# Optimization experiments

Measured on AMD Instinct MI355X. Metric: run time of the kernel, lower is better.

Reference implementation:

```python
import jax, jax.numpy as jnp
import numpy as np

IMG = 800          # image size (square)
STRIDE = 4         # feature-map stride
S = 14             # rcnn_crop_size
C = 256            # crop_channels
N = 512            # number of rpn proposals
NUM_CLASSES = 81   # COCO (incl. background at index 0)
HID = 1024
NMS_TH = 0.5
SCORE_TH = 0.05


def setup_inputs() -> dict:
    key = jax.random.key(0)
    ks = jax.random.split(key, 8)
    features = jax.random.normal(ks[0], (1, C, IMG // STRIDE, IMG // STRIDE), jnp.float32)
    # valid proposal boxes (x0, y0, x1, y1) in image coordinates
    u = jax.random.uniform(ks[1], (N, 4), jnp.float32)
    x0 = u[:, 0] * (IMG - 64.0)
    y0 = u[:, 1] * (IMG - 64.0)
    bw = 16.0 + u[:, 2] * 240.0
    bh = 16.0 + u[:, 3] * 240.0
    proposals = jnp.stack([x0, y0, jnp.minimum(x0 + bw, IMG - 1.0), jnp.minimum(y0 + bh, IMG - 1.0)], axis=1)
    d1 = C * S * S  # 50176
    w1 = jax.random.normal(ks[2], (d1, HID), jnp.float32) * (1.0 / np.sqrt(d1))
    b1 = jnp.zeros((HID,), jnp.float32)
    w2 = jax.random.normal(ks[3], (HID, HID), jnp.float32) * (1.0 / np.sqrt(HID))
    b2 = jnp.zeros((HID,), jnp.float32)
    w_cls = jax.random.normal(ks[4], (HID, NUM_CLASSES), jnp.float32) * (1.0 / np.sqrt(HID))
    b_cls = jnp.zeros((NUM_CLASSES,), jnp.float32)
    w_reg = jax.random.normal(ks[5], (HID, NUM_CLASSES * 4), jnp.float32) * (1.0 / np.sqrt(HID))
    b_reg = jnp.zeros((NUM_CLASSES * 4,), jnp.float32)
    return dict(features=features, proposals=proposals, w1=w1, b1=b1, w2=w2, b2=b2,
                w_cls=w_cls, b_cls=b_cls, w_reg=w_reg, b_reg=b_reg)


def roi_align(feat, boxes):
    """feat: [C,H,W]; boxes: [N,4] image coords -> crops [N,C,S,S] via bilinear sampling (1 sample per bin)."""
    _, H, W = feat.shape
    b = boxes / STRIDE
    t = (jnp.arange(S, dtype=feat.dtype) + 0.5) / S                # [S] bin centers
    xs = b[:, 0:1] + (b[:, 2:3] - b[:, 0:1]) * t                   # [N,S]
    ys = b[:, 1:2] + (b[:, 3:4] - b[:, 1:2]) * t                   # [N,S]
    xx = jnp.broadcast_to(xs[:, None, :], (boxes.shape[0], S, S))  # [N,S,S]
    yy = jnp.broadcast_to(ys[:, :, None], (boxes.shape[0], S, S))
    x0f = jnp.floor(xx); y0f = jnp.floor(yy)
    fx = xx - x0f; fy = yy - y0f
    x0i = jnp.clip(x0f.astype(jnp.int32), 0, W - 1); x1i = jnp.clip(x0i + 1, 0, W - 1)
    y0i = jnp.clip(y0f.astype(jnp.int32), 0, H - 1); y1i = jnp.clip(y0i + 1, 0, H - 1)
    # gathers -> [C,N,S,S]
    v = (((1 - fx) * (1 - fy))[None] * feat[:, y0i, x0i]
         + (fx * (1 - fy))[None] * feat[:, y0i, x1i]
         + ((1 - fx) * fy)[None] * feat[:, y1i, x0i]
         + (fx * fy)[None] * feat[:, y1i, x1i])
    return v.transpose(1, 0, 2, 3)  # [N,C,S,S]


def decode_boxes(rois, d):
    w = rois[:, 2] - rois[:, 0]; h = rois[:, 3] - rois[:, 1]
    cx = rois[:, 0] + 0.5 * w; cy = rois[:, 1] + 0.5 * h
    px = cx + d[:, 0] * w; py = cy + d[:, 1] * h
    pw = w * jnp.exp(jnp.clip(d[:, 2], -4.0, 4.0))
    ph = h * jnp.exp(jnp.clip(d[:, 3], -4.0, 4.0))
    b = jnp.stack([px - 0.5 * pw, py - 0.5 * ph, px + 0.5 * pw, py + 0.5 * ph], axis=1)
    return jnp.clip(b, 0.0, IMG - 1.0)


def iou_matrix(b):
    area = jnp.maximum(b[:, 2] - b[:, 0], 0.0) * jnp.maximum(b[:, 3] - b[:, 1], 0.0)
    ix0 = jnp.maximum(b[:, None, 0], b[None, :, 0])
    iy0 = jnp.maximum(b[:, None, 1], b[None, :, 1])
    ix1 = jnp.minimum(b[:, None, 2], b[None, :, 2])
    iy1 = jnp.minimum(b[:, None, 3], b[None, :, 3])
    inter = jnp.maximum(ix1 - ix0, 0.0) * jnp.maximum(iy1 - iy0, 0.0)
    return inter / (area[:, None] + area[None, :] - inter + 1e-6)


def reference(features, proposals, w1, b1, w2, b2, w_cls, b_cls, w_reg, b_reg):
    # 1) RoIAlign crop
    crops = roi_align(features[0], proposals)              # [N,C,S,S]
    # 2) RCNN head
    x = crops.reshape(N, -1)
    x = jax.nn.relu(x @ w1 + b1)
    x = jax.nn.relu(x @ w2 + b2)
    logits = x @ w_cls + b_cls                             # [N,81]
    deltas = (x @ w_reg + b_reg).reshape(N, NUM_CLASSES, 4)
    # 3) NMS post-processing
    probs = jax.nn.softmax(logits, axis=-1)
    fg = probs[:, 1:]                                      # exclude background
    labels = jnp.argmax(fg, axis=-1) + 1                   # [N]
    scores = jnp.max(fg, axis=-1)                          # [N]
    d = deltas[jnp.arange(N), labels]                      # per-ROI delta of predicted class
    boxes = decode_boxes(proposals, d)
    order = jnp.argsort(-scores)
    bs = boxes[order]; ss = scores[order]; ls = labels[order]
    valid = ss > SCORE_TH
    M = iou_matrix(bs)                                     # [N,N]
    idx = jnp.arange(N)
    def body(i, keep):
        alive = keep[i] & valid[i]
        supp = (M[i] > NMS_TH) & (idx > i) & alive
        return keep & (~supp)
    keep = jax.lax.fori_loop(0, N, body, valid)
    keepf = jax.lax.stop_gradient(keep.astype(bs.dtype))
    final = jnp.concatenate([bs, ss[:, None]], axis=1) * keepf[:, None]   # [N,5]
    return final, ls.astype(jnp.int32), keep
```

## Files before the change

### kernel.cpp

```cpp
#include <hip/hip_runtime.h>
#include <cstdint>

#define F_H 200
#define F_W 200
#define D1  50176
#define NBOX 512
#define NHID 1024

typedef _Float16 f16;
typedef _Float16 half8 __attribute__((ext_vector_type(8)));
typedef _Float16 half4v __attribute__((ext_vector_type(4)));
typedef _Float16 half2v __attribute__((ext_vector_type(2)));
typedef float    f32x4 __attribute__((ext_vector_type(4)));

__device__ __forceinline__ void gload16(const void* g, void* l) {
  __builtin_amdgcn_global_load_lds((const __attribute__((address_space(1))) void*)g,
                                   (__attribute__((address_space(3))) void*)l,
                                   16, 0, 0);
}

__device__ __forceinline__ half2v pkrtz(float a, float b) {
  return __builtin_bit_cast(half2v, __builtin_amdgcn_cvt_pkrtz(a, b));
}

__device__ __forceinline__ void splitf16(float v, f16& h, f16& l) {
  f16 hh = (f16)v;
  float hf = (float)hh;
  if (fabsf(hf) < 6.1035156e-5f) hf = 0.f;
  h = (f16)hh;
  if (fabsf(hf) < 6.1035156e-5f) h = (f16)0.f;
  l = (f16)((v - hf) * 2048.f);
}

__global__ __launch_bounds__(256) void k_roi(const float* __restrict__ feat,
                                             const float* __restrict__ prop,
                                             f16* __restrict__ xhi, f16* __restrict__ xlo) {
  uint32_t idx = blockIdx.x * 256u + threadIdx.x;
  uint32_t n = idx / 25088u;
  uint32_t rem = idx % 25088u;
  uint32_t c = rem / 98u;
  uint32_t r2 = rem % 98u;
  uint32_t i = r2 / 7u;
  uint32_t jp = r2 % 7u;
  float b0 = prop[n * 4 + 0] * 0.25f, b1 = prop[n * 4 + 1] * 0.25f;
  float b2 = prop[n * 4 + 2] * 0.25f, b3 = prop[n * 4 + 3] * 0.25f;
  float ty = ((float)i + 0.5f) * (1.0f / 14.0f);
  float yy = b1 + (b3 - b1) * ty;
  float y0f = floorf(yy);
  float fy = yy - y0f;
  int y0 = (int)y0f; y0 = y0 < 0 ? 0 : (y0 > F_H - 1 ? F_H - 1 : y0);
  int y1 = y0 + 1 > F_H - 1 ? F_H - 1 : y0 + 1;
  const float* fr0 = feat + (size_t)c * (F_H * F_W) + (size_t)y0 * F_W;
  const float* fr1 = feat + (size_t)c * (F_H * F_W) + (size_t)y1 * F_W;
  f16 hs[2], ls[2];
#pragma unroll
  for (int e = 0; e < 2; ++e) {
    uint32_t j = jp * 2u + (uint32_t)e;
    float tx = ((float)j + 0.5f) * (1.0f / 14.0f);
    float xx = b0 + (b2 - b0) * tx;
    float x0f = floorf(xx);
    float fx = xx - x0f;
    int x0 = (int)x0f; x0 = x0 < 0 ? 0 : (x0 > F_W - 1 ? F_W - 1 : x0);
    int x1 = x0 + 1 > F_W - 1 ? F_W - 1 : x0 + 1;
    float v00 = fr0[x0], v01 = fr0[x1], v10 = fr1[x0], v11 = fr1[x1];
    float v = (1.f - fx) * (1.f - fy) * v00 + fx * (1.f - fy) * v01 +
              (1.f - fx) * fy * v10 + fx * fy * v11;
    splitf16(v, hs[e], ls[e]);
  }
  uint32_t base = n * 50176u + c * 196u + i * 14u + jp * 2u;
  half2v hv; hv[0] = hs[0]; hv[1] = hs[1];
  half2v lv; lv[0] = ls[0]; lv[1] = ls[1];
  *(half2v*)(xhi + base) = hv;
  *(half2v*)(xlo + base) = lv;
}

__global__ __launch_bounds__(256) void k_tsplit(const float* __restrict__ W,
                                                f16* __restrict__ hiT, f16* __restrict__ loT,
                                                int Kdim, int Ndim) {
  __shared__ f16 lh[64 * 72];
  __shared__ f16 ll[64 * 72];
  int t = threadIdx.x;
  int k0 = blockIdx.x * 64, n0 = blockIdx.y * 64;
  int r = t >> 2, cq = t & 3;
  const float* src = W + (size_t)(k0 + r) * Ndim + n0 + cq * 16;
  f16 hv[16], lv[16];
#pragma unroll
  for (int e = 0; e < 4; ++e) {
    f32x4 v = *(const f32x4*)(src + e * 4);
#pragma unroll
    for (int x = 0; x < 4; ++x) splitf16(v[x], hv[e * 4 + x], lv[e * 4 + x]);
  }
#pragma unroll
  for (int j = 0; j < 16; ++j) {
    int n_l = cq * 16 + j;
    lh[n_l * 72 + r] = hv[j];
    ll[n_l * 72 + r] = lv[j];
  }
  __syncthreads();
  f16* oh = hiT + (size_t)(n0 + r) * Kdim + k0 + cq * 16;
  f16* ol = loT + (size_t)(n0 + r) * Kdim + k0 + cq * 16;
  *(half8*)(oh)     = *(const half8*)(&lh[r * 72 + cq * 16]);
  *(half8*)(oh + 8) = *(const half8*)(&lh[r * 72 + cq * 16 + 8]);
  *(half8*)(ol)     = *(const half8*)(&ll[r * 72 + cq * 16]);
  *(half8*)(ol + 8) = *(const half8*)(&ll[r * 72 + cq * 16 + 8]);
}

__global__ __launch_bounds__(256) void k_packT(const float* __restrict__ wc_, const float* __restrict__ bc,
                                               const float* __restrict__ wr_, const float* __restrict__ br,
                                               f16* __restrict__ whT_hi, f16* __restrict__ whT_lo,
                                               float* __restrict__ bh) {
  uint32_t idx = blockIdx.x * 256u + threadIdx.x;
  if (idx < 512u * 1024u) {
    uint32_t n = idx >> 10, k = idx & 1023u;
    float v = 0.f;
    if (n < 81u) v = wc_[k * 81u + n];
    else if (n < 405u) v = wr_[k * 324u + (n - 81u)];
    f16 h, l; splitf16(v, h, l);
    whT_hi[idx] = h; whT_lo[idx] = l;
  } else if (idx < 512u * 1024u + 512u) {
    uint32_t n = idx - 512u * 1024u;
    float v = 0.f;
    if (n < 81u) v = bc[n];
    else if (n < 405u) v = br[n - 81u];
    bh[n] = v;
  }
}

__global__ __launch_bounds__(256) void k_pack(const float* __restrict__ wc, const float* __restrict__ bc,
                                              const float* __restrict__ wr, const float* __restrict__ br,
                                              float* __restrict__ wh, float* __restrict__ bh) {
  uint32_t idx = blockIdx.x * 256u + threadIdx.x;
  if (idx < (uint32_t)NHID * 512u) {
    uint32_t k = idx >> 9, n = idx & 511u;
    float v = 0.f;
    if (n < 81u) v = wc[k * 81u + n];
    else if (n < 405u) v = wr[k * 324u + (n - 81u)];
    wh[idx] = v;
  } else if (idx < (uint32_t)NHID * 512u + 512u) {
    uint32_t n = idx - (uint32_t)NHID * 512u;
    float v = 0.f;
    if (n < 81u) v = bc[n];
    else if (n < 405u) v = br[n - 81u];
    bh[n] = v;
  }
}

__global__ __launch_bounds__(512, 2) void k_gemm2(
    const f16* __restrict__ Ahi, const f16* __restrict__ Alo,
    const f16* __restrict__ Bhi, const f16* __restrict__ Blo,
    float* __restrict__ Cp, int K, int N, int Kc, int nMt, int nNt)
{
  __shared__ char sm[131072];
  const int t = threadIdx.x;
  const int lane = t & 63;
  const int wid = t >> 6;
  const int wr = wid >> 2;
  const int wc = wid & 3;
  const int rl = lane & 15;
  const int lq = lane >> 4;

  int bid = blockIdx.x;
  int low = bid & 7, qq = bid >> 3;
  int nt = qq % nNt;
  int chi = qq / nNt;
  int c = chi * 8 + low;
  int ks = c / nMt;
  int mt = c % nMt;
  const int brow = mt * 256;
  const int nbase = nt * 256;
  const int k0 = ks * Kc;
  const int nk = Kc >> 5;

  uint32_t aoffg[2], aldso[2];
#pragma unroll
  for (int i = 0; i < 2; ++i) {
    uint32_t idx = (uint32_t)t + 512u * i;
    uint32_t q2 = idx >> 2, s = idx & 3;
    uint32_t qh = q2 >> 6;
    uint32_t grh = (qh == 1u) ? 2u : (qh == 2u) ? 1u : qh;
    uint32_t gr = grh * 64u + (q2 & 63u);
    aoffg[i] = (uint32_t)(brow + gr) * (uint32_t)K + (s ^ ((q2 >> 1) & 3u)) * 8u;
    aldso[i] = idx * 16u;
  }
  uint32_t boffg[2], bldso[2];
#pragma unroll
  for (int i = 0; i < 2; ++i) {
    uint32_t idx = (uint32_t)t + 512u * i;
    uint32_t rB = idx >> 2, s = idx & 3;
    boffg[i] = (uint32_t)(nbase + rB) * (uint32_t)K + (s ^ ((rB >> 1) & 3u)) * 8u;
    bldso[i] = idx * 16u;
  }

  const uint32_t swzk = (uint32_t)(lq ^ ((rl >> 1) & 3)) * 16u;
  const uint32_t a_off_lane = (uint32_t)(rl * 64) + swzk;
  const uint32_t b_off_lane = (uint32_t)((wc * 16 + rl) * 64) + swzk;

  f32x4 zero4 = {0.f, 0.f, 0.f, 0.f};
  f32x4 acc[8][4];
#pragma unroll
  for (int m = 0; m < 8; ++m)
#pragma unroll
    for (int n = 0; n < 4; ++n) acc[m][n] = zero4;

#define PH0STAGE(LB, KB) do { \
    gload16(Bhi + boffg[0] + (KB), (LB) + 32768 + bldso[0]); \
    gload16(Blo + boffg[0] + (KB), (LB) + 49152 + bldso[0]); \
    gload16(Bhi + boffg[1] + (KB), (LB) + 32768 + bldso[1]); \
    gload16(Blo + boffg[1] + (KB), (LB) + 49152 + bldso[1]); \
    gload16(Ahi + aoffg[0] + (KB), (LB) + aldso[0]); \
    gload16(Alo + aoffg[0] + (KB), (LB) + 16384 + aldso[0]); \
  } while (0)

#define PH1STAGE(LB, KB) do { \
    gload16(Ahi + aoffg[1] + (KB), (LB) + aldso[1]); \
    gload16(Alo + aoffg[1] + (KB), (LB) + 16384 + aldso[1]); \
  } while (0)

#define COMPUTE_PHASE(P) do { \
    half8 bh2[4], bl2[4]; \
    _Pragma("unroll") \
    for (int nf = 0; nf < 4; ++nf) { \
      bh2[nf] = *(const half8*)(lb + 32768 + nf * 4096 + b_off_lane); \
      bl2[nf] = *(const half8*)(lb + 49152 + nf * 4096 + b_off_lane); \
    } \
    __builtin_amdgcn_s_setprio(1); \
    _Pragma("unroll") \
    for (int mm = 0; mm < 4; ++mm) { \
      const char* ab = lb + (P) * 8192 + wr * 4096 + mm * 1024 + a_off_lane; \
      half8 ah = *(const half8*)(ab); \
      half8 al = *(const half8*)(ab + 16384); \
      _Pragma("unroll") \
      for (int nf = 0; nf < 4; ++nf) { \
        acc[(P)*4+mm][nf] = __builtin_amdgcn_mfma_f32_16x16x32_f16(ah, bh2[nf], acc[(P)*4+mm][nf], 0, 0, 0); \
        f32x4 tt = __builtin_amdgcn_mfma_f32_16x16x32_f16(ah, bl2[nf], zero4, 0, 0, 0); \
        tt = __builtin_amdgcn_mfma_f32_16x16x32_f16(al, bh2[nf], tt, 0, 0, 0); \
        acc[(P)*4+mm][nf] += tt * 4.8828125e-4f; \
      } \
    } \
    __builtin_amdgcn_s_setprio(0); \
  } while (0)

  PH0STAGE(sm, (uint32_t)k0);
  PH1STAGE(sm, (uint32_t)k0);

  int cur = 0;
  for (int kt = 0; kt < nk; ++kt) {
    int ktn = (kt + 1 < nk) ? kt + 1 : kt;
    uint32_t kbn = (uint32_t)(k0 + ktn * 32);
    const char* lb = sm + cur * 65536;
    char* lbn = sm + (cur ^ 1) * 65536;

    asm volatile("s_waitcnt vmcnt(2)" ::: "memory");
    __builtin_amdgcn_s_barrier();
    __builtin_amdgcn_sched_barrier(0);
    PH0STAGE(lbn, kbn);
    COMPUTE_PHASE(0);

    asm volatile("s_waitcnt vmcnt(6)" ::: "memory");
    __builtin_amdgcn_s_barrier();
    __builtin_amdgcn_sched_barrier(0);
    PH1STAGE(lbn, kbn);
    COMPUTE_PHASE(1);

    cur ^= 1;
  }

  float* Cs = Cp + (size_t)ks * ((size_t)512 * (uint32_t)N);
#pragma unroll
  for (int m = 0; m < 8; ++m) {
    int rg = brow + wr * 128 + m * 16 + lq * 4;
#pragma unroll
    for (int nf = 0; nf < 4; ++nf) {
      int cg = nbase + nf * 64 + wc * 16 + rl;
#pragma unroll
      for (int rr = 0; rr < 4; ++rr)
        Cs[(size_t)(rg + rr) * (uint32_t)N + cg] = acc[m][nf][rr];
    }
  }
#undef PH0STAGE
#undef PH1STAGE
#undef COMPUTE_PHASE
}

__global__ __launch_bounds__(512, 2) void k_gemm(
    const f16* __restrict__ Ahi, const f16* __restrict__ Alo,
    const float* __restrict__ B, float* __restrict__ Cp,
    int K, int N, int Kc, int nMt, int nNt)
{
  __shared__ char sm[131072];
  const int t = threadIdx.x;
  const int lane = t & 63;
  const int wid = t >> 6;
  const int wr = wid >> 2;
  const int wc = wid & 3;
  const int rl = lane & 15;
  const int lq = lane >> 4;

  int bid = blockIdx.x;
  int low = bid & 7, q = bid >> 3;
  int nt = q % nNt;
  int chi = q / nNt;
  int c = chi * 8 + low;
  int ks = c / nMt;
  int mt = c % nMt;
  const int brow = mt * 256;
  const int nbase = nt * 256;
  const int k0 = ks * Kc;
  const int nk = Kc >> 5;

  uint32_t aoffg[2], aldso[2];
#pragma unroll
  for (int i = 0; i < 2; ++i) {
    uint32_t idx = (uint32_t)t + 512u * i;
    uint32_t r = idx >> 2, s = idx & 3;
    uint32_t sz = s ^ ((r >> 1) & 3);
    aoffg[i] = (uint32_t)(brow + r) * (uint32_t)K + sz * 8u;
    aldso[i] = idx * 16u;
  }
  uint32_t boffg[2][2], bldso[2][2];
#pragma unroll
  for (int h = 0; h < 2; ++h)
#pragma unroll
    for (int i = 0; i < 2; ++i) {
      uint32_t idx = (uint32_t)t + 512u * i;
      uint32_t kr = idx >> 5, sg = idx & 31;
      uint32_t sgs = sg ^ (((kr >> 3) & 3) << 2);
      boffg[h][i] = kr * (uint32_t)N + (uint32_t)(nbase + h * 128) + sgs * 4u;
      bldso[h][i] = 32768u + (uint32_t)h * 16384u + idx * 16u;
    }

  const uint32_t a_off = (uint32_t)(wr * 8192 + rl * 64) + (uint32_t)((lq ^ ((rl >> 1) & 3)) * 16);
  const uint32_t b_lane = (uint32_t)((((wc ^ lq) & 3) * 16 + rl) * 4);

  f32x4 zero4 = {0.f, 0.f, 0.f, 0.f};
  f32x4 acc[8][4];
#pragma unroll
  for (int m = 0; m < 8; ++m)
#pragma unroll
    for (int n = 0; n < 4; ++n) acc[m][n] = zero4;

#define STAGE_A(LB, KB) do { \
    gload16(Ahi + aoffg[0] + (KB), (LB) + aldso[0]); \
    gload16(Alo + aoffg[0] + (KB), (LB) + 16384 + aldso[0]); \
    gload16(Ahi + aoffg[1] + (KB), (LB) + aldso[1]); \
    gload16(Alo + aoffg[1] + (KB), (LB) + 16384 + aldso[1]); \
  } while (0)

#define STAGE_B(LB, KB) do { \
    gload16(B + (size_t)(KB) * (uint32_t)N + boffg[0][0], (LB) + bldso[0][0]); \
    gload16(B + (size_t)(KB) * (uint32_t)N + boffg[0][1], (LB) + bldso[0][1]); \
    gload16(B + (size_t)(KB) * (uint32_t)N + boffg[1][0], (LB) + bldso[1][0]); \
    gload16(B + (size_t)(KB) * (uint32_t)N + boffg[1][1], (LB) + bldso[1][1]); \
  } while (0)

#define COMPUTE_PHASE(P) do { \
    half8 bhv[2], blv[2]; \
    _Pragma("unroll") \
    for (int x = 0; x < 2; ++x) { \
      const int nf = 2 * (P) + x; \
      const char* bb = lb + 32768 + (nf >> 1) * 16384 + (nf & 1) * 256 + b_lane; \
      _Pragma("unroll") \
      for (int jj = 0; jj < 8; jj += 2) { \
        float v0 = *(const float*)(bb + (lq * 8 + jj) * 512); \
        float v1 = *(const float*)(bb + (lq * 8 + jj + 1) * 512); \
        half2v hp = pkrtz(v0, v1); \
        f16 e0 = (fabsf(v0) >= 6.1035156e-5f) ? hp[0] : (f16)0; \
        f16 e1 = (fabsf(v1) >= 6.1035156e-5f) ? hp[1] : (f16)0; \
        half2v lp = pkrtz((v0 - (float)e0) * 2048.f, (v1 - (float)e1) * 2048.f); \
        bhv[x][jj] = e0; bhv[x][jj + 1] = e1; \
        blv[x][jj] = lp[0]; blv[x][jj + 1] = lp[1]; \
      } \
    } \
    __builtin_amdgcn_s_setprio(1); \
    _Pragma("unroll") \
    for (int m = 0; m < 8; ++m) { \
      half8 ah = *(const half8*)(lb + a_off + m * 1024); \
      half8 al = *(const half8*)(lb + 16384 + a_off + m * 1024); \
      _Pragma("unroll") \
      for (int x = 0; x < 2; ++x) { \
        const int nf = 2 * (P) + x; \
        acc[m][nf] = __builtin_amdgcn_mfma_f32_16x16x32_f16(ah, bhv[x], acc[m][nf], 0, 0, 0); \
        f32x4 tt = __builtin_amdgcn_mfma_f32_16x16x32_f16(ah, blv[x], zero4, 0, 0, 0); \
        tt = __builtin_amdgcn_mfma_f32_16x16x32_f16(al, bhv[x], tt, 0, 0, 0); \
        acc[m][nf] += tt * 4.8828125e-4f; \
      } \
    } \
    __builtin_amdgcn_s_setprio(0); \
  } while (0)

  STAGE_A(sm, (uint32_t)k0);
  STAGE_B(sm, (uint32_t)k0);

  int cur = 0;
  for (int kt = 0; kt < nk; ++kt) {
    int ktn = (kt + 1 < nk) ? kt + 1 : kt;
    uint32_t kbn = (uint32_t)(k0 + ktn * 32);
    const char* lb = sm + cur * 65536;
    char* lbn = sm + (cur ^ 1) * 65536;

    asm volatile("s_waitcnt vmcnt(2)" ::: "memory");
    __builtin_amdgcn_s_barrier();
    __builtin_amdgcn_sched_barrier(0);
    STAGE_A(lbn, kbn);
    COMPUTE_PHASE(0);

    asm volatile("s_waitcnt vmcnt(4)" ::: "memory");
    __builtin_amdgcn_s_barrier();
    __builtin_amdgcn_sched_barrier(0);
    STAGE_B(lbn, kbn);
    COMPUTE_PHASE(1);

    cur ^= 1;
  }

  float* Cs = Cp + (size_t)ks * ((size_t)512 * (uint32_t)N);
#pragma unroll
  for (int m = 0; m < 8; ++m) {
    int rg = brow + wr * 128 + m * 16 + lq * 4;
#pragma unroll
    for (int nf = 0; nf < 4; ++nf) {
      int cg = nbase + nf * 64 + wc * 16 + rl;
#pragma unroll
      for (int rr = 0; rr < 4; ++rr)
        Cs[(size_t)(rg + rr) * (uint32_t)N + cg] = acc[m][nf][rr];
    }
  }
#undef STAGE_A
#undef STAGE_B
#undef COMPUTE_PHASE
}

__global__ __launch_bounds__(256) void k_reduce(
    const float* __restrict__ parts, const float* __restrict__ bias,
    int nS, int MN4, int Ncols, int relu,
    float* __restrict__ outf, f16* __restrict__ ohi, f16* __restrict__ olo)
{
  uint32_t idx = blockIdx.x * 256u + threadIdx.x;
  if (idx >= (uint32_t)MN4) return;
  f32x4 s = *(const f32x4*)(bias + ((idx * 4u) % (uint32_t)Ncols));
  const f32x4* p4 = (const f32x4*)parts;
  for (int i = 0; i < nS; ++i) s += p4[(size_t)i * (uint32_t)MN4 + idx];
  if (relu) {
#pragma unroll
    for (int j = 0; j < 4; ++j) s[j] = fmaxf(s[j], 0.f);
  }
  if (outf) *(f32x4*)(outf + (size_t)idx * 4) = s;
  if (ohi) {
    half4v h, l;
#pragma unroll
    for (int j = 0; j < 4; ++j) { f16 hh, ll; splitf16(s[j], hh, ll); h[j] = hh; l[j] = ll; }
    *(half4v*)(ohi + (size_t)idx * 4) = h;
    *(half4v*)(olo + (size_t)idx * 4) = l;
  }
}

__global__ __launch_bounds__(256) void k_post(
    const float* __restrict__ ld, const float* __restrict__ prop,
    float* __restrict__ boxes, float* __restrict__ scores, int* __restrict__ labels)
{
  int n = blockIdx.x * 256 + threadIdx.x;
  if (n >= NBOX) return;
  const float* L = ld + (size_t)n * 512;
  float m = L[0];
  for (int j = 1; j < 81; ++j) m = fmaxf(m, L[j]);
  float sum = 0.f;
  for (int j = 0; j < 81; ++j) sum += expf(L[j] - m);
  float best = -1.f; int bj = 1;
  for (int j = 1; j < 81; ++j) {
    float p = expf(L[j] - m) / sum;
    if (p > best) { best = p; bj = j; }
  }
  float d0 = L[81 + bj * 4 + 0];
  float d1 = L[81 + bj * 4 + 1];
  float d2 = L[81 + bj * 4 + 2];
  float d3 = L[81 + bj * 4 + 3];
  float p0 = prop[n * 4 + 0], p1 = prop[n * 4 + 1], p2 = prop[n * 4 + 2], p3 = prop[n * 4 + 3];
  float w = p2 - p0, h = p3 - p1;
  float cx = p0 + 0.5f * w, cy = p1 + 0.5f * h;
  float px = cx + d0 * w, py = cy + d1 * h;
  float pw = w * expf(fminf(fmaxf(d2, -4.f), 4.f));
  float ph = h * expf(fminf(fmaxf(d3, -4.f), 4.f));
  float bx0 = px - 0.5f * pw, by0 = py - 0.5f * ph;
  float bx1 = px + 0.5f * pw, by1 = py + 0.5f * ph;
  boxes[n * 4 + 0] = fminf(fmaxf(bx0, 0.f), 799.f);
  boxes[n * 4 + 1] = fminf(fmaxf(by0, 0.f), 799.f);
  boxes[n * 4 + 2] = fminf(fmaxf(bx1, 0.f), 799.f);
  boxes[n * 4 + 3] = fminf(fmaxf(by1, 0.f), 799.f);
  scores[n] = best;
  labels[n] = bj;
}

__global__ __launch_bounds__(512) void k_sort(
    const float* __restrict__ scores, const float* __restrict__ boxes, const int* __restrict__ labels,
    float* __restrict__ bs, float* __restrict__ ss, int* __restrict__ ls)
{
  __shared__ unsigned long long keys[512];
  int t = threadIdx.x;
  unsigned sb = __float_as_uint(scores[t]);
  keys[t] = ((unsigned long long)(0xFFFFFFFFu - sb) << 32) | (unsigned)t;
  __syncthreads();
  for (int k = 2; k <= 512; k <<= 1) {
    for (int j = k >> 1; j > 0; j >>= 1) {
      int p = t ^ j;
      if (p > t) {
        unsigned long long a = keys[t], b = keys[p];
        bool asc = ((t & k) == 0);
        if (asc ? (a > b) : (a < b)) { keys[t] = b; keys[p] = a; }
      }
      __syncthreads();
    }
  }
  unsigned o = (unsigned)(keys[t] & 0xFFFFFFFFu);
  ss[t] = scores[o];
  ls[t] = labels[o];
  bs[t * 4 + 0] = boxes[o * 4 + 0];
  bs[t * 4 + 1] = boxes[o * 4 + 1];
  bs[t * 4 + 2] = boxes[o * 4 + 2];
  bs[t * 4 + 3] = boxes[o * 4 + 3];
}

__global__ __launch_bounds__(64) void k_mask(const float* __restrict__ bs,
                                             unsigned long long* __restrict__ mask) {
  int i = blockIdx.x;
  int lane = threadIdx.x;
  float ax0 = bs[i * 4], ay0 = bs[i * 4 + 1], ax1 = bs[i * 4 + 2], ay1 = bs[i * 4 + 3];
  float aarea = fmaxf(ax1 - ax0, 0.f) * fmaxf(ay1 - ay0, 0.f);
  for (int w = 0; w < 8; ++w) {
    int j = w * 64 + lane;
    float bx0 = bs[j * 4], by0 = bs[j * 4 + 1], bx1 = bs[j * 4 + 2], by1 = bs[j * 4 + 3];
    float barea = fmaxf(bx1 - bx0, 0.f) * fmaxf(by1 - by0, 0.f);
    float ix0 = fmaxf(ax0, bx0), iy0 = fmaxf(ay0, by0);
    float ix1 = fminf(ax1, bx1), iy1 = fminf(ay1, by1);
    float inter = fmaxf(ix1 - ix0, 0.f) * fmaxf(iy1 - iy0, 0.f);
    float iou = inter / (aarea + barea - inter + 1e-6f);
    bool cond = (iou > 0.5f) && (j > i);
    unsigned long long b = __ballot(cond);
    if (lane == 0) mask[i * 8 + w] = b;
  }
}

__global__ __launch_bounds__(64) void k_nms(const unsigned long long* __restrict__ mask,
                                            const float* __restrict__ ss,
                                            const float* __restrict__ bs,
                                            const int* __restrict__ ls,
                                            float* __restrict__ out) {
  int lane = threadIdx.x;
  unsigned long long bal[8];
  for (int w = 0; w < 8; ++w) bal[w] = __ballot(ss[w * 64 + lane] > 0.05f);
  unsigned long long keep = (lane < 8) ? bal[lane] : 0ULL;
  for (int i = 0; i < 512; ++i) {
    unsigned long long kw = __shfl(keep, i >> 6);
    if ((kw >> (i & 63)) & 1ULL) {
      unsigned long long mi = (lane < 8) ? mask[i * 8 + lane] : 0ULL;
      keep &= ~mi;
    }
  }
  __shared__ unsigned long long kws[8];
  if (lane < 8) kws[lane] = keep;
  __syncthreads();
  for (int it = 0; it < 56; ++it) {
    int idx = lane + it * 64;
    float val;
    if (idx < 2560) {
      int i = idx / 5, c2 = idx % 5;
      bool kb = (kws[i >> 6] >> (i & 63)) & 1ULL;
      val = kb ? (c2 < 4 ? bs[i * 4 + c2] : ss[i]) : 0.f;
    } else if (idx < 3072) {
      int i = idx - 2560;
      val = (float)ls[i];
    } else {
      int i = idx - 3072;
      val = ((kws[i >> 6] >> (i & 63)) & 1ULL) ? 1.f : 0.f;
    }
    out[idx] = val;
  }
}

static constexpr size_t SZ_X    = (size_t)NBOX * D1 * 2;
static constexpr size_t OFF_XHI = 0;
static constexpr size_t OFF_XLO = OFF_XHI + SZ_X;
static constexpr size_t OFF_PART = OFF_XLO + SZ_X;
static constexpr size_t SZ_PART = (size_t)32 * 512 * 1024 * 4;
static constexpr size_t SZ_H    = (size_t)512 * 1024 * 2;
static constexpr size_t OFF_H1HI = OFF_PART + SZ_PART;
static constexpr size_t OFF_H1LO = OFF_H1HI + SZ_H;
static constexpr size_t OFF_H2HI = OFF_H1LO + SZ_H;
static constexpr size_t OFF_H2LO = OFF_H2HI + SZ_H;
static constexpr size_t OFF_WH   = OFF_H2LO + SZ_H;
static constexpr size_t OFF_BH   = OFF_WH + (size_t)1024 * 512 * 4;
static constexpr size_t OFF_LD   = OFF_BH + 4096;
static constexpr size_t OFF_BOX  = OFF_LD + (size_t)512 * 512 * 4;
static constexpr size_t OFF_SC   = OFF_BOX + 512 * 4 * 4;
static constexpr size_t OFF_LB   = OFF_SC + 4096;
static constexpr size_t OFF_BS   = OFF_LB + 4096;
static constexpr size_t OFF_SS   = OFF_BS + 512 * 4 * 4;
static constexpr size_t OFF_LS   = OFF_SS + 4096;
static constexpr size_t OFF_MASK = OFF_LS + 4096;
static constexpr size_t OFF_END  = OFF_MASK + (size_t)512 * 8 * 8;

static constexpr size_t SZ_W1P   = (size_t)1024 * D1 * 2;
static constexpr size_t NP_XHI   = 0;
static constexpr size_t NP_XLO   = NP_XHI + SZ_X;
static constexpr size_t NP_W1HIT = NP_XLO + SZ_X;
static constexpr size_t NP_W1LOT = NP_W1HIT + SZ_W1P;
static constexpr size_t NP_PART  = NP_W1LOT + SZ_W1P;
static constexpr size_t NP_W2HIT = NP_PART + SZ_PART;
static constexpr size_t NP_W2LOT = NP_W2HIT + (size_t)1024 * 1024 * 2;
static constexpr size_t NP_WHHIT = NP_W2LOT + (size_t)1024 * 1024 * 2;
static constexpr size_t NP_WHLOT = NP_WHHIT + (size_t)512 * 1024 * 2;
static constexpr size_t NP_BH    = NP_WHLOT + (size_t)512 * 1024 * 2;
static constexpr size_t NP_H1HI  = NP_BH + 4096;
static constexpr size_t NP_H1LO  = NP_H1HI + SZ_H;
static constexpr size_t NP_H2HI  = NP_H1LO + SZ_H;
static constexpr size_t NP_H2LO  = NP_H2HI + SZ_H;
static constexpr size_t NP_LD    = NP_H2LO + SZ_H;
static constexpr size_t NP_BOX   = NP_LD + (size_t)512 * 512 * 4;
static constexpr size_t NP_SC    = NP_BOX + 512 * 4 * 4;
static constexpr size_t NP_LB    = NP_SC + 4096;
static constexpr size_t NP_BS    = NP_LB + 4096;
static constexpr size_t NP_SS    = NP_BS + 512 * 4 * 4;
static constexpr size_t NP_LS    = NP_SS + 4096;
static constexpr size_t NP_MASK  = NP_LS + 4096;
static constexpr size_t NP_END   = NP_MASK + (size_t)512 * 8 * 8;

extern "C" void kernel_launch(void* const* d_in, const int* in_sizes, int n_in,
                              void* d_out, int out_size, void* d_ws, size_t ws_size,
                              hipStream_t stream)
{
  (void)in_sizes; (void)n_in;
  const float* feat = (const float*)d_in[0];
  const float* prop = (const float*)d_in[1];
  const float* w1   = (const float*)d_in[2];
  const float* b1   = (const float*)d_in[3];
  const float* w2   = (const float*)d_in[4];
  const float* b2   = (const float*)d_in[5];
  const float* wcls = (const float*)d_in[6];
  const float* bcls = (const float*)d_in[7];
  const float* wreg = (const float*)d_in[8];
  const float* breg = (const float*)d_in[9];
  float* out = (float*)d_out;
  char* W = (char*)d_ws;

  if (ws_size >= NP_END) {
    f16*   xhi   = (f16*)(W + NP_XHI);
    f16*   xlo   = (f16*)(W + NP_XLO);
    f16*   w1hiT = (f16*)(W + NP_W1HIT);
    f16*   w1loT = (f16*)(W + NP_W1LOT);
    float* parts = (float*)(W + NP_PART);
    f16*   w2hiT = (f16*)(W + NP_W2HIT);
    f16*   w2loT = (f16*)(W + NP_W2LOT);
    f16*   whHiT = (f16*)(W + NP_WHHIT);
    f16*   whLoT = (f16*)(W + NP_WHLOT);
    float* bhead = (float*)(W + NP_BH);
    f16*   h1hi  = (f16*)(W + NP_H1HI);
    f16*   h1lo  = (f16*)(W + NP_H1LO);
    f16*   h2hi  = (f16*)(W + NP_H2HI);
    f16*   h2lo  = (f16*)(W + NP_H2LO);
    float* ldbuf = (float*)(W + NP_LD);
    float* boxes = (float*)(W + NP_BOX);
    float* scores= (float*)(W + NP_SC);
    int*   labels= (int*)(W + NP_LB);
    float* bsrt  = (float*)(W + NP_BS);
    float* ssrt  = (float*)(W + NP_SS);
    int*   lsrt  = (int*)(W + NP_LS);
    unsigned long long* maskb = (unsigned long long*)(W + NP_MASK);

    k_tsplit<<<dim3(D1 / 64, 1024 / 64), 256, 0, stream>>>(w1, w1hiT, w1loT, D1, 1024);
    k_roi<<<50176, 256, 0, stream>>>(feat, prop, xhi, xlo);
    k_tsplit<<<dim3(1024 / 64, 1024 / 64), 256, 0, stream>>>(w2, w2hiT, w2loT, 1024, 1024);
    k_packT<<<2050, 256, 0, stream>>>(wcls, bcls, wreg, breg, whHiT, whLoT, bhead);

    k_gemm2<<<256, 512, 0, stream>>>(xhi, xlo, w1hiT, w1loT, parts, D1, 1024, 1568, 2, 4);
    k_reduce<<<512, 256, 0, stream>>>(parts, b1, 32, 131072, 1024, 1, nullptr, h1hi, h1lo);

    k_gemm2<<<256, 512, 0, stream>>>(h1hi, h1lo, w2hiT, w2loT, parts, 1024, 1024, 32, 2, 4);
    k_reduce<<<512, 256, 0, stream>>>(parts, b2, 32, 131072, 1024, 1, nullptr, h2hi, h2lo);

    k_gemm2<<<128, 512, 0, stream>>>(h2hi, h2lo, whHiT, whLoT, parts, 1024, 512, 32, 2, 2);
    k_reduce<<<256, 256, 0, stream>>>(parts, bhead, 32, 65536, 512, 0, ldbuf, nullptr, nullptr);

    k_post<<<2, 256, 0, stream>>>(ldbuf, prop, boxes, scores, labels);
    k_sort<<<1, 512, 0, stream>>>(scores, boxes, labels, bsrt, ssrt, lsrt);
    k_mask<<<512, 64, 0, stream>>>(bsrt, maskb);
    k_nms<<<1, 64, 0, stream>>>(maskb, ssrt, bsrt, lsrt, out);
    return;
  }

  if (ws_size < OFF_END) {
    (void)hipMemsetAsync(out, 0x7f, (size_t)out_size * 4, stream);
    return;
  }

  f16*   xhi   = (f16*)(W + OFF_XHI);
  f16*   xlo   = (f16*)(W + OFF_XLO);
  float* parts = (float*)(W + OFF_PART);
  f16*   h1hi  = (f16*)(W + OFF_H1HI);
  f16*   h1lo  = (f16*)(W + OFF_H1LO);
  f16*   h2hi  = (f16*)(W + OFF_H2HI);
  f16*   h2lo  = (f16*)(W + OFF_H2LO);
  float* whead = (float*)(W + OFF_WH);
  float* bhead = (float*)(W + OFF_BH);
  float* ldbuf = (float*)(W + OFF_LD);
  float* boxes = (float*)(W + OFF_BOX);
  float* scores= (float*)(W + OFF_SC);
  int*   labels= (int*)(W + OFF_LB);
  float* bsrt  = (float*)(W + OFF_BS);
  float* ssrt  = (float*)(W + OFF_SS);
  int*   lsrt  = (int*)(W + OFF_LS);
  unsigned long long* maskb = (unsigned long long*)(W + OFF_MASK);

  k_pack<<<2050, 256, 0, stream>>>(wcls, bcls, wreg, breg, whead, bhead);
  k_roi<<<50176, 256, 0, stream>>>(feat, prop, xhi, xlo);

  k_gemm<<<256, 512, 0, stream>>>(xhi, xlo, w1, parts, D1, 1024, 1568, 2, 4);
  k_reduce<<<512, 256, 0, stream>>>(parts, b1, 32, 131072, 1024, 1, nullptr, h1hi, h1lo);

  k_gemm<<<64, 512, 0, stream>>>(h1hi, h1lo, w2, parts, 1024, 1024, 128, 2, 4);
  k_reduce<<<512, 256, 0, stream>>>(parts, b2, 8, 131072, 1024, 1, nullptr, h2hi, h2lo);

  k_gemm<<<64, 512, 0, stream>>>(h2hi, h2lo, whead, parts, 1024, 512, 64, 2, 2);
  k_reduce<<<256, 256, 0, stream>>>(parts, bhead, 16, 65536, 512, 0, ldbuf, nullptr, nullptr);

  k_post<<<2, 256, 0, stream>>>(ldbuf, prop, boxes, scores, labels);
  k_sort<<<1, 512, 0, stream>>>(scores, boxes, labels, bsrt, ssrt, lsrt);
  k_mask<<<512, 64, 0, stream>>>(bsrt, maskb);
  k_nms<<<1, 64, 0, stream>>>(maskb, ssrt, bsrt, lsrt, out);
}
```

Measured before the change: 477.9 us.

## Fuse post-processing into one kernel and read fp32 W1 directly in first GEMM

Post-processing (softmax/decode, sort, IoU mask, NMS) moves into a single 512-thread block that keeps boxes, scores and the mask in shared memory, replacing four separate launches and their global round trips. The first GEMM no longer pre-splits the 50176x1024 W1 into transposed fp16 hi/lo copies. It uses the kernel that reads fp32 W1 directly, avoiding a large transpose/split pass over about 200MB of weights. The W2 and head GEMMs keep the pre-split fp16 path. The risk is that the direct-fp32 GEMM is slower than the pre-split one, and the single-block IoU loop is serial per thread.

```diff
diff --git a/kernel.cpp b/kernel.cpp
--- a/kernel.cpp
+++ b/kernel.cpp
@@ -126,25 +126,6 @@
   }
 }
 
-__global__ __launch_bounds__(256) void k_pack(const float* __restrict__ wc, const float* __restrict__ bc,
-                                              const float* __restrict__ wr, const float* __restrict__ br,
-                                              float* __restrict__ wh, float* __restrict__ bh) {
-  uint32_t idx = blockIdx.x * 256u + threadIdx.x;
-  if (idx < (uint32_t)NHID * 512u) {
-    uint32_t k = idx >> 9, n = idx & 511u;
-    float v = 0.f;
-    if (n < 81u) v = wc[k * 81u + n];
-    else if (n < 405u) v = wr[k * 324u + (n - 81u)];
-    wh[idx] = v;
-  } else if (idx < (uint32_t)NHID * 512u + 512u) {
-    uint32_t n = idx - (uint32_t)NHID * 512u;
-    float v = 0.f;
-    if (n < 81u) v = bc[n];
-    else if (n < 405u) v = br[n - 81u];
-    bh[n] = v;
-  }
-}
-
 __global__ __launch_bounds__(512, 2) void k_gemm2(
     const f16* __restrict__ Ahi, const f16* __restrict__ Alo,
     const f16* __restrict__ Bhi, const f16* __restrict__ Blo,
@@ -216,7 +197,7 @@
     gload16(Alo + aoffg[1] + (KB), (LB) + 16384 + aldso[1]); \
   } while (0)
 
-#define COMPUTE_PHASE(P) do { \
+#define COMPUTE_PHASE2(P) do { \
     half8 bh2[4], bl2[4]; \
     _Pragma("unroll") \
     for (int nf = 0; nf < 4; ++nf) { \
@@ -254,13 +235,13 @@
     __builtin_amdgcn_s_barrier();
     __builtin_amdgcn_sched_barrier(0);
     PH0STAGE(lbn, kbn);
-    COMPUTE_PHASE(0);
+    COMPUTE_PHASE2(0);
 
     asm volatile("s_waitcnt vmcnt(6)" ::: "memory");
     __builtin_amdgcn_s_barrier();
     __builtin_amdgcn_sched_barrier(0);
     PH1STAGE(lbn, kbn);
-    COMPUTE_PHASE(1);
+    COMPUTE_PHASE2(1);
 
     cur ^= 1;
   }
@@ -279,10 +260,10 @@
   }
 #undef PH0STAGE
 #undef PH1STAGE
-#undef COMPUTE_PHASE
-}
-
-__global__ __launch_bounds__(512, 2) void k_gemm(
+#undef COMPUTE_PHASE2
+}
+
+__global__ __launch_bounds__(512, 2) void k_gemm3(
     const f16* __restrict__ Ahi, const f16* __restrict__ Alo,
     const float* __restrict__ B, float* __restrict__ Cp,
     int K, int N, int Kc, int nMt, int nNt)
@@ -454,50 +435,52 @@
   }
 }
 
-__global__ __launch_bounds__(256) void k_post(
+__global__ __launch_bounds__(512) void k_tail(
     const float* __restrict__ ld, const float* __restrict__ prop,
-    float* __restrict__ boxes, float* __restrict__ scores, int* __restrict__ labels)
+    float* __restrict__ out)
 {
-  int n = blockIdx.x * 256 + threadIdx.x;
-  if (n >= NBOX) return;
-  const float* L = ld + (size_t)n * 512;
-  float m = L[0];
-  for (int j = 1; j < 81; ++j) m = fmaxf(m, L[j]);
-  float sum = 0.f;
-  for (int j = 0; j < 81; ++j) sum += expf(L[j] - m);
-  float best = -1.f; int bj = 1;
-  for (int j = 1; j < 81; ++j) {
-    float p = expf(L[j] - m) / sum;
-    if (p > best) { best = p; bj = j; }
-  }
-  float d0 = L[81 + bj * 4 + 0];
-  float d1 = L[81 + bj * 4 + 1];
-  float d2 = L[81 + bj * 4 + 2];
-  float d3 = L[81 + bj * 4 + 3];
-  float p0 = prop[n * 4 + 0], p1 = prop[n * 4 + 1], p2 = prop[n * 4 + 2], p3 = prop[n * 4 + 3];
-  float w = p2 - p0, h = p3 - p1;
-  float cx = p0 + 0.5f * w, cy = p1 + 0.5f * h;
-  float px = cx + d0 * w, py = cy + d1 * h;
-  float pw = w * expf(fminf(fmaxf(d2, -4.f), 4.f));
-  float ph = h * expf(fminf(fmaxf(d3, -4.f), 4.f));
-  float bx0 = px - 0.5f * pw, by0 = py - 0.5f * ph;
-  float bx1 = px + 0.5f * pw, by1 = py + 0.5f * ph;
-  boxes[n * 4 + 0] = fminf(fmaxf(bx0, 0.f), 799.f);
-  boxes[n * 4 + 1] = fminf(fmaxf(by0, 0.f), 799.f);
-  boxes[n * 4 + 2] = fminf(fmaxf(bx1, 0.f), 799.f);
-  boxes[n * 4 + 3] = fminf(fmaxf(by1, 0.f), 799.f);
-  scores[n] = best;
-  labels[n] = bj;
-}
-
-__global__ __launch_bounds__(512) void k_sort(
-    const float* __restrict__ scores, const float* __restrict__ boxes, const int* __restrict__ labels,
-    float* __restrict__ bs, float* __restrict__ ss, int* __restrict__ ls)
-{
+  __shared__ float sbox[512][4];
+  __shared__ float ssc[512];
+  __shared__ int   slb[512];
   __shared__ unsigned long long keys[512];
+  __shared__ unsigned long long maskw[512][8];
+  __shared__ unsigned long long kws[8];
   int t = threadIdx.x;
-  unsigned sb = __float_as_uint(scores[t]);
-  keys[t] = ((unsigned long long)(0xFFFFFFFFu - sb) << 32) | (unsigned)t;
+
+  {
+    const float* L = ld + (size_t)t * 512;
+    float m = L[0];
+    for (int j = 1; j < 81; ++j) m = fmaxf(m, L[j]);
+    float sum = 0.f;
+    for (int j = 0; j < 81; ++j) sum += expf(L[j] - m);
+    float best = -1.f; int bj = 1;
+    for (int j = 1; j < 81; ++j) {
+      float p = expf(L[j] - m) / sum;
+      if (p > best) { best = p; bj = j; }
+    }
+    float d0 = L[81 + bj * 4 + 0];
+    float d1 = L[81 + bj * 4 + 1];
+    float d2 = L[81 + bj * 4 + 2];
+    float d3 = L[81 + bj * 4 + 3];
+    float p0 = prop[t * 4 + 0], p1 = prop[t * 4 + 1], p2 = prop[t * 4 + 2], p3 = prop[t * 4 + 3];
+    float w = p2 - p0, h = p3 - p1;
+    float cx = p0 + 0.5f * w, cy = p1 + 0.5f * h;
+    float px = cx + d0 * w, py = cy + d1 * h;
+    float pw = w * expf(fminf(fmaxf(d2, -4.f), 4.f));
+    float ph = h * expf(fminf(fmaxf(d3, -4.f), 4.f));
+    sbox[t][0] = fminf(fmaxf(px - 0.5f * pw, 0.f), 799.f);
+    sbox[t][1] = fminf(fmaxf(py - 0.5f * ph, 0.f), 799.f);
+    sbox[t][2] = fminf(fmaxf(px + 0.5f * pw, 0.f), 799.f);
+    sbox[t][3] = fminf(fmaxf(py + 0.5f * ph, 0.f), 799.f);
+    ssc[t] = best;
+    slb[t] = bj;
+  }
+  __syncthreads();
+
+  {
+    unsigned sb = __float_as_uint(ssc[t]);
+    keys[t] = ((unsigned long long)(0xFFFFFFFFu - sb) << 32) | (unsigned)t;
+  }
   __syncthreads();
   for (int k = 2; k <= 512; k <<= 1) {
     for (int j = k >> 1; j > 0; j >>= 1) {
@@ -511,63 +494,59 @@
     }
   }
   unsigned o = (unsigned)(keys[t] & 0xFFFFFFFFu);
-  ss[t] = scores[o];
-  ls[t] = labels[o];
-  bs[t * 4 + 0] = boxes[o * 4 + 0];
-  bs[t * 4 + 1] = boxes[o * 4 + 1];
-  bs[t * 4 + 2] = boxes[o * 4 + 2];
-  bs[t * 4 + 3] = boxes[o * 4 + 3];
-}
-
-__global__ __launch_bounds__(64) void k_mask(const float* __restrict__ bs,
-                                             unsigned long long* __restrict__ mask) {
-  int i = blockIdx.x;
-  int lane = threadIdx.x;
-  float ax0 = bs[i * 4], ay0 = bs[i * 4 + 1], ax1 = bs[i * 4 + 2], ay1 = bs[i * 4 + 3];
-  float aarea = fmaxf(ax1 - ax0, 0.f) * fmaxf(ay1 - ay0, 0.f);
-  for (int w = 0; w < 8; ++w) {
-    int j = w * 64 + lane;
-    float bx0 = bs[j * 4], by0 = bs[j * 4 + 1], bx1 = bs[j * 4 + 2], by1 = bs[j * 4 + 3];
-    float barea = fmaxf(bx1 - bx0, 0.f) * fmaxf(by1 - by0, 0.f);
-    float ix0 = fmaxf(ax0, bx0), iy0 = fmaxf(ay0, by0);
-    float ix1 = fminf(ax1, bx1), iy1 = fminf(ay1, by1);
-    float inter = fmaxf(ix1 - ix0, 0.f) * fmaxf(iy1 - iy0, 0.f);
-    float iou = inter / (aarea + barea - inter + 1e-6f);
-    bool cond = (iou > 0.5f) && (j > i);
-    unsigned long long b = __ballot(cond);
-    if (lane == 0) mask[i * 8 + w] = b;
-  }
-}
-
-__global__ __launch_bounds__(64) void k_nms(const unsigned long long* __restrict__ mask,
-                                            const float* __restrict__ ss,
-                                            const float* __restrict__ bs,
-                                            const int* __restrict__ ls,
-                                            float* __restrict__ out) {
-  int lane = threadIdx.x;
-  unsigned long long bal[8];
-  for (int w = 0; w < 8; ++w) bal[w] = __ballot(ss[w * 64 + lane] > 0.05f);
-  unsigned long long keep = (lane < 8) ? bal[lane] : 0ULL;
-  for (int i = 0; i < 512; ++i) {
-    unsigned long long kw = __shfl(keep, i >> 6);
-    if ((kw >> (i & 63)) & 1ULL) {
-      unsigned long long mi = (lane < 8) ? mask[i * 8 + lane] : 0ULL;
-      keep &= ~mi;
-    }
-  }
-  __shared__ unsigned long long kws[8];
-  if (lane < 8) kws[lane] = keep;
+  float g0 = sbox[o][0], g1 = sbox[o][1], g2 = sbox[o][2], g3 = sbox[o][3];
+  float gs = ssc[o]; int gl = slb[o];
   __syncthreads();
-  for (int it = 0; it < 56; ++it) {
-    int idx = lane + it * 64;
+  sbox[t][0] = g0; sbox[t][1] = g1; sbox[t][2] = g2; sbox[t][3] = g3;
+  ssc[t] = gs; slb[t] = gl;
+  __syncthreads();
+
+  {
+    float ax0 = sbox[t][0], ay0 = sbox[t][1], ax1 = sbox[t][2], ay1 = sbox[t][3];
+    float aarea = fmaxf(ax1 - ax0, 0.f) * fmaxf(ay1 - ay0, 0.f);
+    for (int w = 0; w < 8; ++w) {
+      unsigned long long bits = 0ULL;
+      for (int l = 0; l < 64; ++l) {
+        int j = w * 64 + l;
+        float bx0 = sbox[j][0], by0 = sbox[j][1], bx1 = sbox[j][2], by1 = sbox[j][3];
+        float barea = fmaxf(bx1 - bx0, 0.f) * fmaxf(by1 - by0, 0.f);
+        float ix0 = fmaxf(ax0, bx0), iy0 = fmaxf(ay0, by0);
+        float ix1 = fminf(ax1, bx1), iy1 = fminf(ay1, by1);
+        float inter = fmaxf(ix1 - ix0, 0.f) * fmaxf(iy1 - iy0, 0.f);
+        float iou = inter / (aarea + barea - inter + 1e-6f);
+        if ((iou > 0.5f) && (j > t)) bits |= (1ULL << l);
+      }
+      maskw[t][w] = bits;
+    }
+  }
+  __syncthreads();
+
+  if (t < 64) {
+    int lane = t;
+    unsigned long long bal[8];
+    for (int w = 0; w < 8; ++w) bal[w] = __ballot(ssc[w * 64 + lane] > 0.05f);
+    unsigned long long keep = (lane < 8) ? bal[lane] : 0ULL;
+    for (int i = 0; i < 512; ++i) {
+      unsigned long long kw = __shfl(keep, i >> 6);
+      if ((kw >> (i & 63)) & 1ULL) {
+        unsigned long long mi = (lane < 8) ? maskw[i][lane] : 0ULL;
+        keep &= ~mi;
+      }
+    }
+    if (lane < 8) kws[lane] = keep;
+  }
+  __syncthreads();
+
+  for (int it = 0; it < 7; ++it) {
+    int idx = t + it * 512;
     float val;
     if (idx < 2560) {
       int i = idx / 5, c2 = idx % 5;
       bool kb = (kws[i >> 6] >> (i & 63)) & 1ULL;
-      val = kb ? (c2 < 4 ? bs[i * 4 + c2] : ss[i]) : 0.f;
+      val = kb ? (c2 < 4 ? sbox[i][c2] : ssc[i]) : 0.f;
     } else if (idx < 3072) {
       int i = idx - 2560;
-      val = (float)ls[i];
+      val = (float)slb[i];
     } else {
       int i = idx - 3072;
       val = ((kws[i >> 6] >> (i & 63)) & 1ULL) ? 1.f : 0.f;
@@ -577,33 +556,11 @@
 }
 
 static constexpr size_t SZ_X    = (size_t)NBOX * D1 * 2;
-static constexpr size_t OFF_XHI = 0;
-static constexpr size_t OFF_XLO = OFF_XHI + SZ_X;
-static constexpr size_t OFF_PART = OFF_XLO + SZ_X;
 static constexpr size_t SZ_PART = (size_t)32 * 512 * 1024 * 4;
 static constexpr size_t SZ_H    = (size_t)512 * 1024 * 2;
-static constexpr size_t OFF_H1HI = OFF_PART + SZ_PART;
-static constexpr size_t OFF_H1LO = OFF_H1HI + SZ_H;
-static constexpr size_t OFF_H2HI = OFF_H1LO + SZ_H;
-static constexpr size_t OFF_H2LO = OFF_H2HI + SZ_H;
-static constexpr size_t OFF_WH   = OFF_H2LO + SZ_H;
-static constexpr size_t OFF_BH   = OFF_WH + (size_t)1024 * 512 * 4;
-static constexpr size_t OFF_LD   = OFF_BH + 4096;
-static constexpr size_t OFF_BOX  = OFF_LD + (size_t)512 * 512 * 4;
-static constexpr size_t OFF_SC   = OFF_BOX + 512 * 4 * 4;
-static constexpr size_t OFF_LB   = OFF_SC + 4096;
-static constexpr size_t OFF_BS   = OFF_LB + 4096;
-static constexpr size_t OFF_SS   = OFF_BS + 512 * 4 * 4;
-static constexpr size_t OFF_LS   = OFF_SS + 4096;
-static constexpr size_t OFF_MASK = OFF_LS + 4096;
-static constexpr size_t OFF_END  = OFF_MASK + (size_t)512 * 8 * 8;
-
-static constexpr size_t SZ_W1P   = (size_t)1024 * D1 * 2;
 static constexpr size_t NP_XHI   = 0;
 static constexpr size_t NP_XLO   = NP_XHI + SZ_X;
-static constexpr size_t NP_W1HIT = NP_XLO + SZ_X;
-static constexpr size_t NP_W1LOT = NP_W1HIT + SZ_W1P;
-static constexpr size_t NP_PART  = NP_W1LOT + SZ_W1P;
+static constexpr size_t NP_PART  = NP_XLO + SZ_X;
 static constexpr size_t NP_W2HIT = NP_PART + SZ_PART;
 static constexpr size_t NP_W2LOT = NP_W2HIT + (size_t)1024 * 1024 * 2;
 static constexpr size_t NP_WHHIT = NP_W2LOT + (size_t)1024 * 1024 * 2;
@@ -614,14 +571,7 @@
 static constexpr size_t NP_H2HI  = NP_H1LO + SZ_H;
 static constexpr size_t NP_H2LO  = NP_H2HI + SZ_H;
 static constexpr size_t NP_LD    = NP_H2LO + SZ_H;
-static constexpr size_t NP_BOX   = NP_LD + (size_t)512 * 512 * 4;
-static constexpr size_t NP_SC    = NP_BOX + 512 * 4 * 4;
-static constexpr size_t NP_LB    = NP_SC + 4096;
-static constexpr size_t NP_BS    = NP_LB + 4096;
-static constexpr size_t NP_SS    = NP_BS + 512 * 4 * 4;
-static constexpr size_t NP_LS    = NP_SS + 4096;
-static constexpr size_t NP_MASK  = NP_LS + 4096;
-static constexpr size_t NP_END   = NP_MASK + (size_t)512 * 8 * 8;
+static constexpr size_t NP_END   = NP_LD + (size_t)512 * 512 * 4;
 
 extern "C" void kernel_launch(void* const* d_in, const int* in_sizes, int n_in,
                               void* d_out, int out_size, void* d_ws, size_t ws_size,
@@ -641,88 +591,37 @@
   float* out = (float*)d_out;
   char* W = (char*)d_ws;
 
-  if (ws_size >= NP_END) {
-    f16*   xhi   = (f16*)(W + NP_XHI);
-    f16*   xlo   = (f16*)(W + NP_XLO);
-    f16*   w1hiT = (f16*)(W + NP_W1HIT);
-    f16*   w1loT = (f16*)(W + NP_W1LOT);
-    float* parts = (float*)(W + NP_PART);
-    f16*   w2hiT = (f16*)(W + NP_W2HIT);
-    f16*   w2loT = (f16*)(W + NP_W2LOT);
-    f16*   whHiT = (f16*)(W + NP_WHHIT);
-    f16*   whLoT = (f16*)(W + NP_WHLOT);
-    float* bhead = (float*)(W + NP_BH);
-    f16*   h1hi  = (f16*)(W + NP_H1HI);
-    f16*   h1lo  = (f16*)(W + NP_H1LO);
-    f16*   h2hi  = (f16*)(W + NP_H2HI);
-    f16*   h2lo  = (f16*)(W + NP_H2LO);
-    float* ldbuf = (float*)(W + NP_LD);
-    float* boxes = (float*)(W + NP_BOX);
-    float* scores= (float*)(W + NP_SC);
-    int*   labels= (int*)(W + NP_LB);
-    float* bsrt  = (float*)(W + NP_BS);
-    float* ssrt  = (float*)(W + NP_SS);
-    int*   lsrt  = (int*)(W + NP_LS);
-    unsigned long long* maskb = (unsigned long long*)(W + NP_MASK);
-
-    k_tsplit<<<dim3(D1 / 64, 1024 / 64), 256, 0, stream>>>(w1, w1hiT, w1loT, D1, 1024);
-    k_roi<<<50176, 256, 0, stream>>>(feat, prop, xhi, xlo);
-    k_tsplit<<<dim3(1024 / 64, 1024 / 64), 256, 0, stream>>>(w2, w2hiT, w2loT, 1024, 1024);
-    k_packT<<<2050, 256, 0, stream>>>(wcls, bcls, wreg, breg, whHiT, whLoT, bhead);
-
-    k_gemm2<<<256, 512, 0, stream>>>(xhi, xlo, w1hiT, w1loT, parts, D1, 1024, 1568, 2, 4);
-    k_reduce<<<512, 256, 0, stream>>>(parts, b1, 32, 131072, 1024, 1, nullptr, h1hi, h1lo);
-
-    k_gemm2<<<256, 512, 0, stream>>>(h1hi, h1lo, w2hiT, w2loT, parts, 1024, 1024, 32, 2, 4);
-    k_reduce<<<512, 256, 0, stream>>>(parts, b2, 32, 131072, 1024, 1, nullptr, h2hi, h2lo);
-
-    k_gemm2<<<128, 512, 0, stream>>>(h2hi, h2lo, whHiT, whLoT, parts, 1024, 512, 32, 2, 2);
-    k_reduce<<<256, 256, 0, stream>>>(parts, bhead, 32, 65536, 512, 0, ldbuf, nullptr, nullptr);
-
-    k_post<<<2, 256, 0, stream>>>(ldbuf, prop, boxes, scores, labels);
-    k_sort<<<1, 512, 0, stream>>>(scores, boxes, labels, bsrt, ssrt, lsrt);
-    k_mask<<<512, 64, 0, stream>>>(bsrt, maskb);
-    k_nms<<<1, 64, 0, stream>>>(maskb, ssrt, bsrt, lsrt, out);
-    return;
-  }
-
-  if (ws_size < OFF_END) {
+  if (ws_size < NP_END) {
     (void)hipMemsetAsync(out, 0x7f, (size_t)out_size * 4, stream);
     return;
   }
 
-  f16*   xhi   = (f16*)(W + OFF_XHI);
-  f16*   xlo   = (f16*)(W + OFF_XLO);
-  float* parts = (float*)(W + OFF_PART);
-  f16*   h1hi  = (f16*)(W + OFF_H1HI);
-  f16*   h1lo  = (f16*)(W + OFF_H1LO);
-  f16*   h2hi  = (f16*)(W + OFF_H2HI);
-  f16*   h2lo  = (f16*)(W + OFF_H2LO);
-  float* whead = (float*)(W + OFF_WH);
-  float* bhead = (float*)(W + OFF_BH);
-  float* ldbuf = (float*)(W + OFF_LD);
-  float* boxes = (float*)(W + OFF_BOX);
-  float* scores= (float*)(W + OFF_SC);
-  int*   labels= (int*)(W + OFF_LB);
-  float* bsrt  = (float*)(W + OFF_BS);
-  float* ssrt  = (float*)(W + OFF_SS);
-  int*   lsrt  = (int*)(W + OFF_LS);
-  unsigned long long* maskb = (unsigned long long*)(W + OFF_MASK);
-
-  k_pack<<<2050, 256, 0, stream>>>(wcls, bcls, wreg, breg, whead, bhead);
+  f16*   xhi   = (f16*)(W + NP_XHI);
+  f16*   xlo   = (f16*)(W + NP_XLO);
+  float* parts = (float*)(W + NP_PART);
+  f16*   w2hiT = (f16*)(W + NP_W2HIT);
+  f16*   w2loT = (f16*)(W + NP_W2LOT);
+  f16*   whHiT = (f16*)(W + NP_WHHIT);
+  f16*   whLoT = (f16*)(W + NP_WHLOT);
+  float* bhead = (float*)(W + NP_BH);
+  f16*   h1hi  = (f16*)(W + NP_H1HI);
+  f16*   h1lo  = (f16*)(W + NP_H1LO);
+  f16*   h2hi  = (f16*)(W + NP_H2HI);
+  f16*   h2lo  = (f16*)(W + NP_H2LO);
+  float* ldbuf = (float*)(W + NP_LD);
+
   k_roi<<<50176, 256, 0, stream>>>(feat, prop, xhi, xlo);
-
-  k_gemm<<<256, 512, 0, stream>>>(xhi, xlo, w1, parts, D1, 1024, 1568, 2, 4);
+  k_tsplit<<<dim3(1024 / 64, 1024 / 64), 256, 0, stream>>>(w2, w2hiT, w2loT, 1024, 1024);
+  k_packT<<<2050, 256, 0, stream>>>(wcls, bcls, wreg, breg, whHiT, whLoT, bhead);
+
+  k_gemm3<<<256, 512, 0, stream>>>(xhi, xlo, w1, parts, D1, 1024, 1568, 2, 4);
   k_reduce<<<512, 256, 0, stream>>>(parts, b1, 32, 131072, 1024, 1, nullptr, h1hi, h1lo);
 
-  k_gemm<<<64, 512, 0, stream>>>(h1hi, h1lo, w2, parts, 1024, 1024, 128, 2, 4);
-  k_reduce<<<512, 256, 0, stream>>>(parts, b2, 8, 131072, 1024, 1, nullptr, h2hi, h2lo);
-
-  k_gemm<<<64, 512, 0, stream>>>(h2hi, h2lo, whead, parts, 1024, 512, 64, 2, 2);
-  k_reduce<<<256, 256, 0, stream>>>(parts, bhead, 16, 65536, 512, 0, ldbuf, nullptr, nullptr);
-
-  k_post<<<2, 256, 0, stream>>>(ldbuf, prop, boxes, scores, labels);
-  k_sort<<<1, 512, 0, stream>>>(scores, boxes, labels, bsrt, ssrt, lsrt);
-  k_mask<<<512, 64, 0, stream>>>(bsrt, maskb);
-  k_nms<<<1, 64, 0, stream>>>(maskb, ssrt, bsrt, lsrt, out);
-}
+  k_gemm2<<<256, 512, 0, stream>>>(h1hi, h1lo, w2hiT, w2loT, parts, 1024, 1024, 32, 2, 4);
+  k_reduce<<<512, 256, 0, stream>>>(parts, b2, 32, 131072, 1024, 1, nullptr, h2hi, h2lo);
+
+  k_gemm2<<<128, 512, 0, stream>>>(h2hi, h2lo, whHiT, whLoT, parts, 1024, 512, 32, 2, 2);
+  k_reduce<<<256, 256, 0, stream>>>(parts, bhead, 32, 65536, 512, 0, ldbuf, nullptr, nullptr);
+
+  k_tail<<<1, 512, 0, stream>>>(ldbuf, prop, out);
+}
```

Result: no change. 483.2 us (+1.1%).
